# Optimization experiments

Measured on AMD Instinct MI355X. Metric: run time of the kernel, lower is better.

The kernel has to match this reference:

```python
import jax, jax.numpy as jnp
import numpy as np

CAPACITY = 60.0
CONS_RATE = 0.2
T_LIMIT = 11.0
VELOCITY = 60.0
NUM_AFS = 3
BS, SEQ, H = 256, 256, 128
NEG = -1e9


def setup_inputs() -> dict:
    key = jax.random.key(0)
    ks = jax.random.split(key, 12)
    coords = jax.random.uniform(ks[0], (BS, SEQ, 2))
    static = jnp.transpose(coords, (0, 2, 1))  # [bs, 2, seq]
    diff = coords[:, :, None, :] - coords[:, None, :, :]
    distances = jnp.sqrt(jnp.sum(diff * diff, -1) + 1e-12)  # [bs, seq, seq]
    demands = jax.random.uniform(ks[1], (BS, SEQ), minval=0.1, maxval=1.0)
    demands = demands.at[:, :NUM_AFS + 1].set(0.0)  # depot + AFS have no demand
    dynamic = jnp.stack([jnp.full((BS, SEQ), CAPACITY),
                         jnp.full((BS, SEQ), T_LIMIT),
                         demands], axis=1)  # [bs, 3, seq]
    p = lambda k, shape: 0.1 * jax.random.normal(k, shape)
    return dict(
        static=static, dynamic=dynamic, distances=distances,
        W_s=p(ks[2], (H, 2)), b_s=jnp.zeros(H),
        W_d=p(ks[3], (H, 3)), b_d=jnp.zeros(H),
        W_i=p(ks[4], (4 * H, H)), W_h=p(ks[5], (4 * H, H)),
        b_i=jnp.zeros(4 * H), b_h=jnp.zeros(4 * H),
        W_att=p(ks[6], (H, 3 * H)), v_att=p(ks[7], (H,)),
        W_c=p(ks[8], (H, 2 * H)), b_c=jnp.zeros(H),
        decode_steps=128)


def reference(static, dynamic, distances, W_s, b_s, W_d, b_d, W_i, W_h, b_i, b_h,
              W_att, v_att, W_c, b_c, decode_steps):
    bs, _, seq = static.shape
    h = W_s.shape[0]
    arange_b = jnp.arange(bs)
    node_ids = jnp.arange(seq)

    # Encoder = Conv1d(kernel=1): [bs,c,seq] -> [bs,h,seq]
    stat_emb = jnp.einsum('oc,bcs->bos', W_s, static) + b_s[None, :, None]

    # dis_by_afs: cheapest via-AFS distance from each node to depot
    dba = jnp.stack([distances[:, i, 0:1] + distances[:, i, :]
                     for i in range(1, NUM_AFS + 1)], 1)  # [bs, num_afs, seq]
    dis_by_afs = jnp.min(dba, axis=1).at[:, 0].set(0.0)    # [bs, seq]

    fuel0 = dynamic[:, 0, 0]
    time0 = dynamic[:, 1, 0]
    dem0 = dynamic[:, 2, :]
    ones_seq = jnp.ones((1, seq), static.dtype)

    def enc_dyn(fuel, time, dem):
        dyn = jnp.stack([fuel[:, None] * ones_seq, time[:, None] * ones_seq, dem], 1)
        return jnp.einsum('oc,bcs->bos', W_d, dyn) + b_d[None, :, None]

    def step(carry, key):
        fuel, time, dem, hst, cst, old_idx, dec_in, mask = carry
        dyn_emb = enc_dyn(fuel, time, dem)
        # one LSTM step (PyTorch gate order i,f,g,o)
        gates = dec_in @ W_i.T + hst @ W_h.T + b_i + b_h
        ig, fg, gg, og = jnp.split(gates, 4, axis=-1)
        cst = jax.nn.sigmoid(fg) * cst + jax.nn.sigmoid(ig) * jnp.tanh(gg)
        h_lstm = jax.nn.sigmoid(og) * jnp.tanh(cst)
        # pointer attention over nodes
        feat = jnp.concatenate(
            [stat_emb, dyn_emb, jnp.broadcast_to(h_lstm[:, :, None], (bs, h, seq))], axis=1)
        e = jnp.einsum('k,bks->bs', v_att,
                       jnp.tanh(jnp.einsum('kc,bcs->bks', W_att, feat)))
        logits = jnp.where(mask, e, NEG)
        idx = jax.random.categorical(key, logits)               # sample next node
        logp = jax.nn.log_softmax(logits)[arange_b, idx]
        probs = jax.nn.softmax(logits)
        context = jnp.einsum('bs,bhs->bh', probs, stat_emb)
        h_new = jnp.tanh(jnp.concatenate([context, h_lstm], -1) @ W_c.T + b_c)
        # update_fn: fuel/time/demand dynamics + feasibility mask
        dis = distances[arange_b, old_idx, idx]
        fuel = fuel - CONS_RATE * dis
        time = time - dis / VELOCITY
        at_dep = idx == 0
        at_af = (idx >= 1) & (idx <= NUM_AFS)
        fuel = jnp.where(at_dep | at_af, CAPACITY, fuel)
        time = jnp.where(at_dep, T_LIMIT, time)
        dem = dem.at[arange_b, idx].set(jnp.where(idx > NUM_AFS, 0.0, dem[arange_b, idx]))
        d_next = distances[arange_b, idx, :]  # [bs, seq]
        fuel_ok = fuel[:, None] >= CONS_RATE * (d_next + dis_by_afs)
        time_ok = time[:, None] >= (d_next + distances[:, :, 0]) / VELOCITY
        cust_mask = (dem > 0) & fuel_ok & time_ok
        depot_af_mask = node_ids[None, :] != idx[:, None]
        mask = jnp.where(node_ids[None, :] <= NUM_AFS, depot_af_mask, cust_mask)
        mask = mask.at[:, 0].set(True)  # depot always reachable -> no all-masked rows
        dec_in = stat_emb[arange_b, :, idx]
        return (fuel, time, dem, h_new, cst, idx, dec_in, mask), (probs, idx, logp)

    init = (fuel0, time0, dem0,
            jnp.zeros((bs, h)), jnp.zeros((bs, h)),
            jnp.zeros(bs, jnp.int32), stat_emb[:, :, 0],
            jnp.ones((bs, seq), bool))
    keys = jax.random.split(jax.random.key(1), decode_steps)
    _, (probs, tours, logps) = jax.lax.scan(step, init, keys)
    # outputs [bs, T, seq], tours [bs, T], tour_logp [bs, T]
    return jnp.transpose(probs, (1, 0, 2)), tours.T, logps.T
```

## Files before the change

### kernel.cpp

```cpp
#include <hip/hip_runtime.h>
#include <cmath>

#define BSZ 256
#define SEQN 256
#define HD 128
#define NEGV -1000000000.0f
#define TINYF 1.17549435e-38f
#define LOG2E 1.4426950408889634f
#define LN2F 0.6931471805599453f

typedef float v2f __attribute__((ext_vector_type(2)));

static __device__ __forceinline__ v2f mk2(float a, float b) {
  v2f r; r.x = a; r.y = b; return r;
}
static __device__ __forceinline__ v2f fma2(v2f a, v2f b, v2f c) {
  return __builtin_elementwise_fma(a, b, c);
}

#define DPPF(x, c) __int_as_float(__builtin_amdgcn_update_dpp(0, __float_as_int(x), (c), 0xF, 0xF, true))
#define DPPI(x, c) __builtin_amdgcn_update_dpp(0, (x), (c), 0xF, 0xF, true)
#define SWZF(x, p) __int_as_float(__builtin_amdgcn_ds_swizzle(__float_as_int(x), (p)))

static __device__ __forceinline__ void tf2x32(unsigned k0, unsigned k1,
                                              unsigned x0, unsigned x1,
                                              unsigned &o0, unsigned &o1) {
  unsigned ks2 = k0 ^ k1 ^ 0x1BD11BDAu;
#define TFR(r) { x0 += x1; x1 = (x1 << (r)) | (x1 >> (32 - (r))); x1 ^= x0; }
  x0 += k0; x1 += k1;
  TFR(13) TFR(15) TFR(26) TFR(6)
  x0 += k1; x1 += ks2 + 1u;
  TFR(17) TFR(29) TFR(16) TFR(24)
  x0 += ks2; x1 += k0 + 2u;
  TFR(13) TFR(15) TFR(26) TFR(6)
  x0 += k0; x1 += k1 + 3u;
  TFR(17) TFR(29) TFR(16) TFR(24)
  x0 += k1; x1 += ks2 + 4u;
  TFR(13) TFR(15) TFR(26) TFR(6)
  x0 += ks2; x1 += k0 + 5u;
#undef TFR
  o0 = x0; o1 = x1;
}

static __device__ __forceinline__ float fast_tanh(float x) {
  float y = __fmul_rn(x, 2.885390081777927f);
  float ay = __int_as_float(__float_as_int(y) | 0x80000000u);
  float q = __builtin_amdgcn_exp2f(ay);
  float r = __fmul_rn(__fsub_rn(1.0f, q),
                      __builtin_amdgcn_rcpf(__fadd_rn(1.0f, q)));
  unsigned sgn = (unsigned)__float_as_int(x) & 0x80000000u;
  return __int_as_float(__float_as_int(r) | sgn);
}

static __device__ __forceinline__ float fast_sig(float x) {
  float q = __builtin_amdgcn_exp2f(__fmul_rn(x, -LOG2E));
  return __builtin_amdgcn_rcpf(__fadd_rn(1.0f, q));
}

static __device__ __forceinline__ float fast_ln(float x) {
  return __fmul_rn(__builtin_amdgcn_logf(x), LN2F);
}

static __device__ __forceinline__ v2f tanh2(v2f x) {
  v2f y = x * mk2(2.885390081777927f, 2.885390081777927f);
  y = __builtin_elementwise_min(y, mk2(48.0f, 48.0f));
  v2f s; s.x = __builtin_amdgcn_exp2f(y.x); s.y = __builtin_amdgcn_exp2f(y.y);
  v2f n = s + mk2(-1.0f, -1.0f);
  v2f d = s + mk2(1.0f, 1.0f);
  v2f r; r.x = __builtin_amdgcn_rcpf(d.x); r.y = __builtin_amdgcn_rcpf(d.y);
  return n * r;
}

__global__ __launch_bounds__(512, 2) void evrp_kernel(
    const float* __restrict__ statc, const float* __restrict__ dyn,
    const float* __restrict__ dist,  const float* __restrict__ W_s,
    const float* __restrict__ b_s,   const float* __restrict__ W_d,
    const float* __restrict__ b_d,   const float* __restrict__ W_i,
    const float* __restrict__ W_h,   const float* __restrict__ b_i,
    const float* __restrict__ b_h,   const float* __restrict__ W_att,
    const float* __restrict__ v_att, const float* __restrict__ W_c,
    const float* __restrict__ b_c,   const int* __restrict__ steps_p,
    float* __restrict__ out) {
  const int b = blockIdx.x;
  const int tid = threadIdx.x;
  const int T = steps_p[0];
  const int lane = tid & 63;
  const int wv = tid >> 6;
  const int s = tid >> 1, hf = tid & 1;
  const int cq = tid >> 2, g = tid & 3;

  extern __shared__ __align__(16) float4 Pdyn[];

  __shared__ __align__(16) float  B0a[HD], B1a[HD], A2a[HD];
  __shared__ __align__(16) float  Ct[HD], Vt[HD];
  __shared__ __align__(16) float  hstm[HD], hlm[HD], wc2v[HD];
  __shared__ __align__(16) float  A0a[HD], A1a[HD], D0a[HD];
  __shared__ __align__(16) float  C0a[HD], C1a[HD], C2a[HD], bca[HD];
  __shared__ __align__(16) float2 xy2[SEQN];
  __shared__ __align__(16) float  drowX[SEQN];
  __shared__ __align__(16) unsigned kAs[256], kBs[256];
  __shared__ __align__(16) float ws0[HD], ws1[HD], bsv[HD];
  __shared__ __align__(16) float wd0[HD], wd1[HD], wd2[HD], bdv[HD];
  __shared__ __align__(16) float2 wredA[8];
  __shared__ __align__(16) float4 wredB[8];

  const float* distb = dist + (size_t)b * SEQN * SEQN;

  if (tid < HD) {
    ws0[tid] = W_s[2 * tid]; ws1[tid] = W_s[2 * tid + 1]; bsv[tid] = b_s[tid];
    wd0[tid] = W_d[3 * tid]; wd1[tid] = W_d[3 * tid + 1]; wd2[tid] = W_d[3 * tid + 2];
    bdv[tid] = b_d[tid]; bca[tid] = b_c[tid];
    hstm[tid] = 0.0f;
  }
  float xreg = statc[b * 2 * SEQN + s];
  float yreg = statc[b * 2 * SEQN + SEQN + s];
  float demreg = dyn[b * 3 * SEQN + 2 * SEQN + s];
  float d2dR = distb[(size_t)s * SEQN];
  float dbaR;
  {
    float d10 = distb[1 * SEQN + 0], d20 = distb[2 * SEQN + 0], d30 = distb[3 * SEQN + 0];
    float d1s = distb[1 * SEQN + s], d2s = distb[2 * SEQN + s], d3s = distb[3 * SEQN + s];
    float m = fminf(fminf(__fadd_rn(d10, d1s), __fadd_rn(d20, d2s)), __fadd_rn(d30, d3s));
    dbaR = (s == 0) ? 0.0f : m;
  }
  float dnextR = distb[s];
  if (hf == 0) xy2[s] = make_float2(xreg, yreg);
  float fuelR = dyn[b * 3 * SEQN + 0];
  float timeR = dyn[b * 3 * SEQN + SEQN + 0];
  float cstR = 0.0f;
  int niR = 0;
  for (int tt = tid; tt < 256; tt += 512) {
    unsigned a0, a1; tf2x32(0u, 1u, 0u, (unsigned)tt, a0, a1);
    kAs[tt] = a0; kBs[tt] = a1;
  }
  __syncthreads();

  if (tid < HD) {
    int k = tid;
    const float* row = W_att + (size_t)k * 384;
    float B0 = 0, B1 = 0, B2 = 0, A0 = 0, A1 = 0, A2 = 0, A3 = 0;
    for (int c = 0; c < HD; ++c) {
      float w1 = row[c], w2 = row[128 + c];
      B0 = fmaf(w1, ws0[c], B0); B1 = fmaf(w1, ws1[c], B1); B2 = fmaf(w1, bsv[c], B2);
      A0 = fmaf(w2, wd0[c], A0); A1 = fmaf(w2, wd1[c], A1);
      A2 = fmaf(w2, wd2[c], A2); A3 = fmaf(w2, bdv[c], A3);
    }
    B0a[k] = B0; B1a[k] = B1; A2a[k] = A2; Vt[k] = v_att[k];
    A0a[k] = A0; A1a[k] = A1; D0a[k] = __fadd_rn(B2, A3);
  } else if (tid < 2 * HD) {
    int o = tid - HD;
    const float* row = W_c + (size_t)o * 256;
    float C0 = 0, C1 = 0, C2 = 0;
    for (int c = 0; c < HD; ++c) {
      float w = row[c];
      C0 = fmaf(w, ws0[c], C0); C1 = fmaf(w, ws1[c], C1); C2 = fmaf(w, bsv[c], C2);
    }
    C0a[o] = C0; C1a[o] = C1; C2a[o] = C2;
  }
  float gp0 = 0, gp1 = 0, gp2 = 0, gpw;
  {
    int j = g * HD + cq;
    const float* row = W_i + (size_t)j * HD;
    for (int c = 0; c < HD; ++c) {
      float w = row[c];
      gp0 = fmaf(w, ws0[c], gp0); gp1 = fmaf(w, ws1[c], gp1); gp2 = fmaf(w, bsv[c], gp2);
    }
    gpw = __fadd_rn(b_i[j], b_h[j]);
  }
  v2f whreg2[HD / 2];
  {
    int j = g * HD + cq;
#pragma unroll
    for (int c2 = 0; c2 < HD / 2; ++c2)
      whreg2[c2] = *(const v2f*)(&W_h[(size_t)j * HD + 2 * c2]);
  }
  v2f wah2[16], wc22[16];
#pragma unroll
  for (int i = 0; i < 16; ++i) {
    wah2[i] = *(const v2f*)(&W_att[(size_t)cq * 384 + 256 + g * 32 + 2 * i]);
    wc22[i] = *(const v2f*)(&W_c[(size_t)cq * 256 + HD + g * 32 + 2 * i]);
  }
#pragma unroll
  for (int c = 0; c < HD / 2; c += 2)
    asm volatile("" : "+v"(whreg2[c]), "+v"(whreg2[c + 1]));
#pragma unroll
  for (int i = 0; i < 16; i += 2) {
    asm volatile("" : "+v"(wah2[i]), "+v"(wah2[i + 1]));
    asm volatile("" : "+v"(wc22[i]), "+v"(wc22[i + 1]));
  }
  __syncthreads();

  for (int idx = tid; idx < SEQN * HD; idx += 512) {
    int ss = idx >> 7, k = idx & 127;
    float2 pxy = xy2[ss];
    float dm = dyn[b * 3 * SEQN + 2 * SEQN + ss];
    float pv = fmaf(B0a[k], pxy.x, fmaf(B1a[k], pxy.y, __fmul_rn(A2a[k], dm)));
    ((float*)Pdyn)[(((k >> 2) & 15) << 11) + ((ss * 2 + (k >> 6)) << 2) + (k & 3)] = pv;
  }
  __syncthreads();

  float decxR = xy2[0].x, decyR = xy2[0].y;

  float* out_probs = out;
  float* out_tours = out + (size_t)BSZ * T * SEQN;
  float* out_logps = out_tours + (size_t)BSZ * T;

  const float4* Pp = Pdyn + (s * 2 + hf);
  const float* CtH = Ct + hf * 64;
  const float* VtH = Vt + hf * 64;

  float prevPr = 0.0f, prevLp = 0.0f;
  int prevNi = 0;

  for (int t = 0; t < T; ++t) {
    if (t > 0) {
      if (hf == 0) out_probs[((size_t)b * T + (t - 1)) * SEQN + s] = prevPr;
      if (s == prevNi && hf == 0) {
        out_tours[(size_t)b * T + (t - 1)] = (float)prevNi;
        out_logps[(size_t)b * T + (t - 1)] = prevLp;
      }
      dnextR = distb[(size_t)niR * SEQN + s];
    }
    {
      v2f mA = mk2(0.f, 0.f), mB = mk2(0.f, 0.f);
      const float4* h4 = (const float4*)hstm;
#pragma unroll
      for (int c4 = 0; c4 < HD / 4; ++c4) {
        float4 hh = h4[c4];
        mA = fma2(whreg2[2 * c4],     mk2(hh.x, hh.y), mA);
        mB = fma2(whreg2[2 * c4 + 1], mk2(hh.z, hh.w), mB);
      }
      float md = fmaf(gp0, decxR, fmaf(gp1, decyR, gp2));
      float mh = __fadd_rn(__fadd_rn(mA.x, mA.y), __fadd_rn(mB.x, mB.y));
      float V = __fadd_rn(__fadd_rn(md, mh), gpw);
      float sg = fast_sig(V), th = fast_tanh(V);
      float q = (g == 2) ? th : sg;
      float u1 = DPPF(q, 0xB1);
      float u2 = DPPF(q, 0x4E);
      float u3 = DPPF(q, 0x1B);
      float qi = (g == 0) ? q  : (g == 1) ? u1 : (g == 2) ? u2 : u3;
      float qf = (g == 0) ? u1 : (g == 1) ? q  : (g == 2) ? u3 : u2;
      float qg = (g == 0) ? u2 : (g == 1) ? u3 : (g == 2) ? q  : u1;
      float qo = (g == 0) ? u3 : (g == 1) ? u2 : (g == 2) ? u1 : q;
      float cn = __fadd_rn(__fmul_rn(qf, cstR), __fmul_rn(qi, qg));
      cstR = cn;
      float hv = __fmul_rn(qo, fast_tanh(cn));
      if (g == 0) hlm[(cq & 96) | ((cq & 31) ^ ((cq >> 5) << 3))] = hv;
    }
    __syncthreads();
    {
      v2f pwA = mk2(0.f, 0.f), pwB = mk2(0.f, 0.f);
      v2f pcA = mk2(0.f, 0.f), pcB = mk2(0.f, 0.f);
      const float4* hl4 = (const float4*)hlm;
#pragma unroll
      for (int l4 = 0; l4 < 8; ++l4) {
        float4 hh = hl4[(g << 3) + (l4 ^ (g << 1))];
        v2f hA = mk2(hh.x, hh.y), hB = mk2(hh.z, hh.w);
        pwA = fma2(wah2[2 * l4],     hA, pwA);
        pwB = fma2(wah2[2 * l4 + 1], hB, pwB);
        pcA = fma2(wc22[2 * l4],     hA, pcA);
        pcB = fma2(wc22[2 * l4 + 1], hB, pcB);
      }
      float pw = __fadd_rn(__fadd_rn(pwA.x, pwA.y), __fadd_rn(pwB.x, pwB.y));
      float pc = __fadd_rn(__fadd_rn(pcA.x, pcA.y), __fadd_rn(pcB.x, pcB.y));
      pw = __fadd_rn(pw, DPPF(pw, 0xB1));
      pc = __fadd_rn(pc, DPPF(pc, 0xB1));
      pw = __fadd_rn(pw, DPPF(pw, 0x4E));
      pc = __fadd_rn(pc, DPPF(pc, 0x4E));
      if (g == 0) {
        wc2v[cq] = pc;
        Ct[cq] = fmaf(A0a[cq], fuelR, fmaf(A1a[cq], timeR, __fadd_rn(D0a[cq], pw)));
      }
    }
    __syncthreads();
    float pe, lg;
    if (hf == 0) drowX[s] = dnextR;
    bool mk;
    if (t == 0) mk = true;
    else {
      bool fok = fuelR >= __fmul_rn(0.2f, __fadd_rn(dnextR, dbaR));
      bool tok = timeR >= __fdiv_rn(__fadd_rn(dnextR, d2dR), 60.0f);
      bool cust = (demreg > 0.0f) && fok && tok;
      mk = (s <= 3) ? (s != niR) : cust;
      if (s == 0) mk = true;
    }
    {
      unsigned rb;
      { unsigned o0, o1; tf2x32(kAs[t], kBs[t], 0u, (unsigned)(b * SEQN + s), o0, o1); rb = o0 ^ o1; }
      float f = __uint_as_float((rb >> 9) | 0x3f800000u) - 1.0f;
      float u = fmaxf(TINYF, __fadd_rn(f, TINYF));
      float gmb = -fast_ln(-fast_ln(u));
      v2f acc2 = mk2(0.f, 0.f);
#pragma unroll
      for (int i = 0; i < 16; ++i) {
        float4 pv = Pp[i << 9];
        float4 ct = *(const float4*)(CtH + 4 * i);
        float4 vv = *(const float4*)(VtH + 4 * i);
        v2f a0 = mk2(pv.x, pv.y) + mk2(ct.x, ct.y);
        acc2 = fma2(mk2(vv.x, vv.y), tanh2(a0), acc2);
        v2f a1 = mk2(pv.z, pv.w) + mk2(ct.z, ct.w);
        acc2 = fma2(mk2(vv.z, vv.w), tanh2(a1), acc2);
      }
      float acc = __fadd_rn(acc2.x, acc2.y);
      float e = __fadd_rn(acc, DPPF(acc, 0xB1));
      lg = mk ? e : NEGV;
      pe = __builtin_amdgcn_exp2f(__fmul_rn(lg, LOG2E));
      float sc = __fadd_rn(gmb, lg);
      float av = sc; int ai = s;
      float S = pe, px = __fmul_rn(pe, xreg), py = __fmul_rn(pe, yreg);
      {
        float ov = DPPF(av, 0x4E); int oi = DPPI(ai, 0x4E);
        if (ov > av || (ov == av && oi < ai)) { av = ov; ai = oi; }
        S  = __fadd_rn(S,  DPPF(S,  0x4E));
        px = __fadd_rn(px, DPPF(px, 0x4E));
        py = __fadd_rn(py, DPPF(py, 0x4E));
      }
      {
        float ov = DPPF(av, 0x124); int oi = DPPI(ai, 0x124);
        if (ov > av || (ov == av && oi < ai)) { av = ov; ai = oi; }
        S  = __fadd_rn(S,  DPPF(S,  0x124));
        px = __fadd_rn(px, DPPF(px, 0x124));
        py = __fadd_rn(py, DPPF(py, 0x124));
      }
      {
        float ov = DPPF(av, 0x128); int oi = DPPI(ai, 0x128);
        if (ov > av || (ov == av && oi < ai)) { av = ov; ai = oi; }
        S  = __fadd_rn(S,  DPPF(S,  0x128));
        px = __fadd_rn(px, DPPF(px, 0x128));
        py = __fadd_rn(py, DPPF(py, 0x128));
      }
      {
        float ov = SWZF(av, 0x401F); int oi = __builtin_amdgcn_ds_swizzle(ai, 0x401F);
        if (ov > av || (ov == av && oi < ai)) { av = ov; ai = oi; }
        S  = __fadd_rn(S,  SWZF(S,  0x401F));
        px = __fadd_rn(px, SWZF(px, 0x401F));
        py = __fadd_rn(py, SWZF(py, 0x401F));
      }
      {
        float ov = __shfl_xor(av, 32, 64); int oi = __shfl_xor(ai, 32, 64);
        if (ov > av || (ov == av && oi < ai)) { av = ov; ai = oi; }
        S  = __fadd_rn(S,  __shfl_xor(S,  32, 64));
        px = __fadd_rn(px, __shfl_xor(px, 32, 64));
        py = __fadd_rn(py, __shfl_xor(py, 32, 64));
      }
      if (lane == 0) {
        wredA[wv] = make_float2(av, (float)ai);
        wredB[wv] = make_float4(S, px, py, 0.0f);
      }
    }
    __syncthreads();
    {
      float2 a0 = wredA[0];
      float bv = a0.x; int bi = (int)a0.y;
#pragma unroll
      for (int w = 1; w < 8; ++w) {
        float2 aw = wredA[w];
        if (aw.x > bv) { bv = aw.x; bi = (int)aw.y; }
      }
      int ni = bi;
      float4 b0 = wredB[0];
      float S = b0.x, px = b0.y, py = b0.z;
#pragma unroll
      for (int w = 1; w < 8; ++w) {
        float4 bw = wredB[w];
        S = __fadd_rn(S, bw.x); px = __fadd_rn(px, bw.y); py = __fadd_rn(py, bw.z);
      }
      float dis = drowX[ni];
      float fl = __fsub_rn(fuelR, __fmul_rn(0.2f, dis));
      float tm = __fsub_rn(timeR, __fdiv_rn(dis, 60.0f));
      if (ni <= 3) fl = 60.0f;
      if (ni == 0) tm = 11.0f;
      fuelR = fl; timeR = tm;
      if (s == ni && ni > 3) demreg = 0.0f;
      float2 dxy = xy2[ni];
      decxR = dxy.x; decyR = dxy.y;
      prevPr = __fdiv_rn(pe, S);
      prevLp = __fsub_rn(lg, fast_ln(S));
      prevNi = ni;
      if (tid < HD) {
        float cx = __fdiv_rn(px, S), cy = __fdiv_rn(py, S);
        float ctxd = fmaf(C0a[tid], cx, fmaf(C1a[tid], cy, C2a[tid]));
        float val = __fadd_rn(__fadd_rn(ctxd, wc2v[tid]), bca[tid]);
        hstm[tid] = fast_tanh(val);
      }
      niR = ni;
    }
    __syncthreads();
  }
  if (hf == 0) out_probs[((size_t)b * T + (T - 1)) * SEQN + s] = prevPr;
  if (s == prevNi && hf == 0) {
    out_tours[(size_t)b * T + (T - 1)] = (float)prevNi;
    out_logps[(size_t)b * T + (T - 1)] = prevLp;
  }
}

extern "C" void kernel_launch(void* const* d_in, const int* in_sizes, int n_in,
                              void* d_out, int out_size, void* d_ws, size_t ws_size,
                              hipStream_t stream) {
  (void)in_sizes; (void)n_in; (void)out_size; (void)d_ws; (void)ws_size;
  (void)hipFuncSetAttribute((const void*)evrp_kernel,
                            hipFuncAttributeMaxDynamicSharedMemorySize,
                            SEQN * HD * 4);
  evrp_kernel<<<dim3(BSZ), dim3(512), SEQN * HD * 4, stream>>>(
      (const float*)d_in[0],  (const float*)d_in[1],  (const float*)d_in[2],
      (const float*)d_in[3],  (const float*)d_in[4],  (const float*)d_in[5],
      (const float*)d_in[6],  (const float*)d_in[7],  (const float*)d_in[8],
      (const float*)d_in[9],  (const float*)d_in[10], (const float*)d_in[11],
      (const float*)d_in[12], (const float*)d_in[13], (const float*)d_in[14],
      (const int*)d_in[15],   (float*)d_out);
}
```

Before: 853.2 us.

## Factor attention tanh into precomputed exponentials to cut per-step transcendentals

After: 747.2 us (median of 2 runs). 12.4% less time.

```diff
diff --git a/kernel.cpp b/kernel.cpp
--- a/kernel.cpp
+++ b/kernel.cpp
@@ -8,6 +8,7 @@
 #define TINYF 1.17549435e-38f
 #define LOG2E 1.4426950408889634f
 #define LN2F 0.6931471805599453f
+#define K2L 2.885390081777927f
 
 typedef float v2f __attribute__((ext_vector_type(2)));
 
@@ -43,7 +44,7 @@
 }
 
 static __device__ __forceinline__ float fast_tanh(float x) {
-  float y = __fmul_rn(x, 2.885390081777927f);
+  float y = __fmul_rn(x, K2L);
   float ay = __int_as_float(__float_as_int(y) | 0x80000000u);
   float q = __builtin_amdgcn_exp2f(ay);
   float r = __fmul_rn(__fsub_rn(1.0f, q),
@@ -59,16 +60,6 @@
 
 static __device__ __forceinline__ float fast_ln(float x) {
   return __fmul_rn(__builtin_amdgcn_logf(x), LN2F);
-}
-
-static __device__ __forceinline__ v2f tanh2(v2f x) {
-  v2f y = x * mk2(2.885390081777927f, 2.885390081777927f);
-  y = __builtin_elementwise_min(y, mk2(48.0f, 48.0f));
-  v2f s; s.x = __builtin_amdgcn_exp2f(y.x); s.y = __builtin_amdgcn_exp2f(y.y);
-  v2f n = s + mk2(-1.0f, -1.0f);
-  v2f d = s + mk2(1.0f, 1.0f);
-  v2f r; r.x = __builtin_amdgcn_rcpf(d.x); r.y = __builtin_amdgcn_rcpf(d.y);
-  return n * r;
 }
 
 __global__ __launch_bounds__(512, 2) void evrp_kernel(
@@ -195,7 +186,14 @@
     float2 pxy = xy2[ss];
     float dm = dyn[b * 3 * SEQN + 2 * SEQN + ss];
     float pv = fmaf(B0a[k], pxy.x, fmaf(B1a[k], pxy.y, __fmul_rn(A2a[k], dm)));
-    ((float*)Pdyn)[(((k >> 2) & 15) << 11) + ((ss * 2 + (k >> 6)) << 2) + (k & 3)] = pv;
+    ((float*)Pdyn)[(((k >> 2) & 15) << 11) + ((ss * 2 + (k >> 6)) << 2) + (k & 3)] =
+        __builtin_amdgcn_exp2f(__fmul_rn(pv, K2L));
+  }
+  float Vsum = 0.0f;
+#pragma unroll
+  for (int i = 0; i < 32; ++i) {
+    float4 v4 = ((const float4*)Vt)[i];
+    Vsum = __fadd_rn(Vsum, __fadd_rn(__fadd_rn(v4.x, v4.y), __fadd_rn(v4.z, v4.w)));
   }
   __syncthreads();
 
@@ -222,16 +220,21 @@
       dnextR = distb[(size_t)niR * SEQN + s];
     }
     {
-      v2f mA = mk2(0.f, 0.f), mB = mk2(0.f, 0.f);
+      v2f mA0 = mk2(0.f, 0.f), mB0 = mk2(0.f, 0.f);
+      v2f mA1 = mk2(0.f, 0.f), mB1 = mk2(0.f, 0.f);
       const float4* h4 = (const float4*)hstm;
 #pragma unroll
-      for (int c4 = 0; c4 < HD / 4; ++c4) {
-        float4 hh = h4[c4];
-        mA = fma2(whreg2[2 * c4],     mk2(hh.x, hh.y), mA);
-        mB = fma2(whreg2[2 * c4 + 1], mk2(hh.z, hh.w), mB);
+      for (int c8 = 0; c8 < HD / 8; ++c8) {
+        float4 h0 = h4[2 * c8], h1 = h4[2 * c8 + 1];
+        mA0 = fma2(whreg2[4 * c8 + 0], mk2(h0.x, h0.y), mA0);
+        mB0 = fma2(whreg2[4 * c8 + 1], mk2(h0.z, h0.w), mB0);
+        mA1 = fma2(whreg2[4 * c8 + 2], mk2(h1.x, h1.y), mA1);
+        mB1 = fma2(whreg2[4 * c8 + 3], mk2(h1.z, h1.w), mB1);
       }
       float md = fmaf(gp0, decxR, fmaf(gp1, decyR, gp2));
-      float mh = __fadd_rn(__fadd_rn(mA.x, mA.y), __fadd_rn(mB.x, mB.y));
+      float mh = __fadd_rn(
+          __fadd_rn(__fadd_rn(mA0.x, mA0.y), __fadd_rn(mB0.x, mB0.y)),
+          __fadd_rn(__fadd_rn(mA1.x, mA1.y), __fadd_rn(mB1.x, mB1.y)));
       float V = __fadd_rn(__fadd_rn(md, mh), gpw);
       float sg = fast_sig(V), th = fast_tanh(V);
       float q = (g == 2) ? th : sg;
@@ -269,7 +272,8 @@
       pc = __fadd_rn(pc, DPPF(pc, 0x4E));
       if (g == 0) {
         wc2v[cq] = pc;
-        Ct[cq] = fmaf(A0a[cq], fuelR, fmaf(A1a[cq], timeR, __fadd_rn(D0a[cq], pw)));
+        float Ck = fmaf(A0a[cq], fuelR, fmaf(A1a[cq], timeR, __fadd_rn(D0a[cq], pw)));
+        Ct[cq] = __builtin_amdgcn_exp2f(__fmul_rn(Ck, K2L));
       }
     }
     __syncthreads();
@@ -290,19 +294,37 @@
       float f = __uint_as_float((rb >> 9) | 0x3f800000u) - 1.0f;
       float u = fmaxf(TINYF, __fadd_rn(f, TINYF));
       float gmb = -fast_ln(-fast_ln(u));
-      v2f acc2 = mk2(0.f, 0.f);
-#pragma unroll
-      for (int i = 0; i < 16; ++i) {
-        float4 pv = Pp[i << 9];
-        float4 ct = *(const float4*)(CtH + 4 * i);
-        float4 vv = *(const float4*)(VtH + 4 * i);
-        v2f a0 = mk2(pv.x, pv.y) + mk2(ct.x, ct.y);
-        acc2 = fma2(mk2(vv.x, vv.y), tanh2(a0), acc2);
-        v2f a1 = mk2(pv.z, pv.w) + mk2(ct.z, ct.w);
-        acc2 = fma2(mk2(vv.z, vv.w), tanh2(a1), acc2);
-      }
-      float acc = __fadd_rn(acc2.x, acc2.y);
-      float e = __fadd_rn(acc, DPPF(acc, 0xB1));
+      const v2f one2 = mk2(1.0f, 1.0f);
+      v2f a0 = mk2(0.f, 0.f), a1 = mk2(0.f, 0.f);
+      v2f a2 = mk2(0.f, 0.f), a3 = mk2(0.f, 0.f);
+#pragma unroll
+      for (int i = 0; i < 8; ++i) {
+        float4 pv0 = Pp[(2 * i) << 9];
+        float4 ct0 = *(const float4*)(CtH + 8 * i);
+        float4 vv0 = *(const float4*)(VtH + 8 * i);
+        v2f sA = mk2(pv0.x, pv0.y) * mk2(ct0.x, ct0.y) + one2;
+        v2f sB = mk2(pv0.z, pv0.w) * mk2(ct0.z, ct0.w) + one2;
+        v2f rA, rB;
+        rA.x = __builtin_amdgcn_rcpf(sA.x); rA.y = __builtin_amdgcn_rcpf(sA.y);
+        rB.x = __builtin_amdgcn_rcpf(sB.x); rB.y = __builtin_amdgcn_rcpf(sB.y);
+        a0 = fma2(mk2(vv0.x, vv0.y), rA, a0);
+        a1 = fma2(mk2(vv0.z, vv0.w), rB, a1);
+        float4 pv1 = Pp[(2 * i + 1) << 9];
+        float4 ct1 = *(const float4*)(CtH + 8 * i + 4);
+        float4 vv1 = *(const float4*)(VtH + 8 * i + 4);
+        v2f sC = mk2(pv1.x, pv1.y) * mk2(ct1.x, ct1.y) + one2;
+        v2f sD = mk2(pv1.z, pv1.w) * mk2(ct1.z, ct1.w) + one2;
+        v2f rC, rD;
+        rC.x = __builtin_amdgcn_rcpf(sC.x); rC.y = __builtin_amdgcn_rcpf(sC.y);
+        rD.x = __builtin_amdgcn_rcpf(sD.x); rD.y = __builtin_amdgcn_rcpf(sD.y);
+        a2 = fma2(mk2(vv1.x, vv1.y), rC, a2);
+        a3 = fma2(mk2(vv1.z, vv1.w), rD, a3);
+      }
+      v2f t01 = a0 + a1, t23 = a2 + a3;
+      v2f tt = t01 + t23;
+      float part = __fadd_rn(tt.x, tt.y);
+      float tot = __fadd_rn(part, DPPF(part, 0xB1));
+      float e = fmaf(-2.0f, tot, Vsum);
       lg = mk ? e : NEGV;
       pe = __builtin_amdgcn_exp2f(__fmul_rn(lg, LOG2E));
       float sc = __fadd_rn(gmb, lg);
@@ -350,8 +372,8 @@
     }
     __syncthreads();
     {
-      float2 a0 = wredA[0];
-      float bv = a0.x; int bi = (int)a0.y;
+      float2 a0c = wredA[0];
+      float bv = a0c.x; int bi = (int)a0c.y;
 #pragma unroll
       for (int w = 1; w < 8; ++w) {
         float2 aw = wredA[w];
```
